# Kernel optimization log

Measured on AMD Instinct MI355X. Metric: run time of the kernel, lower is better.

Reference implementation:

```python
import jax, jax.numpy as jnp
import numpy as np

B, C = 32768, 1000
EPS = 1e-6

def setup_inputs() -> dict:
    key = jax.random.key(0)
    k1, k2 = jax.random.split(key)
    # p_tar / p_vlm are probability distributions over C classes
    p_tar = jax.nn.softmax(jax.random.normal(k1, (B, C), dtype=jnp.float32), axis=1)
    p_vlm = jax.nn.softmax(jax.random.normal(k2, (B, C), dtype=jnp.float32), axis=1)
    alpha = jnp.array([0.99], dtype=jnp.float32)  # EMA momentum
    memory_bank = jnp.full((C, C), 1.0 / C, dtype=jnp.float32)  # __init__ state
    return {"p_tar": p_tar, "p_vlm": p_vlm, "alpha": alpha, "memory_bank": memory_bank}

def _uncertainty(p):
    return -p * jnp.log(p + EPS)

def reference(p_tar, p_vlm, alpha, memory_bank):
    n_classes = memory_bank.shape[0]
    norm = 1.0 / jnp.sqrt(jnp.float32(n_classes))
    # --- class_prototype_atten (uses PRE-update memory bank, as in torch) ---
    atten = jax.nn.softmax(jnp.matmul(p_tar, memory_bank.T) * norm, axis=1)  # [B, C]
    p_tar_new = jnp.matmul(atten, memory_bank)  # [B, C]
    # --- update_membank: vectorized per-class masked-mean EMA ---
    y_tar = jnp.argmax(p_tar, axis=1)
    y_vlm = jnp.argmax(p_vlm, axis=1)
    agree = y_tar == y_vlm
    # non-agreeing rows dumped into extra segment n_classes
    seg = jnp.where(agree, y_tar, n_classes)
    sums = jax.ops.segment_sum(p_tar, seg, num_segments=n_classes + 1)[:n_classes]  # [C, C]
    counts = jax.ops.segment_sum(agree.astype(p_tar.dtype), seg, num_segments=n_classes + 1)[:n_classes]  # [C]
    has = counts > 0
    mean = sums / jnp.where(has, counts, 1.0)[:, None]
    a = alpha.reshape(())
    bank_new = jnp.where(has[:, None], a * memory_bank + (1.0 - a) * mean, memory_bank)
    # --- uncertainty_mixing ---
    eu_tar = jnp.exp(-_uncertainty(p_tar_new))
    eu_vlm = jnp.exp(-_uncertainty(p_vlm))
    p_mix = (eu_tar * p_tar_new + eu_vlm * p_vlm) / (eu_tar + eu_vlm)
    return p_mix, bank_new
```

## Files before the change

### kernel.cpp

```cpp
#include <hip/hip_runtime.h>
#include <hip/hip_bf16.h>
#include <cstdint>
#include <cstddef>

#define NROWS 32768
#define NCLS  1000
#define KP    1024

typedef unsigned short u16;
typedef __bf16 bf16x8 __attribute__((ext_vector_type(8)));
typedef float  f32x4  __attribute__((ext_vector_type(4)));

__device__ __forceinline__ void gld_lds16(const u16* g, u16* l) {
  __builtin_amdgcn_global_load_lds(
      (const __attribute__((address_space(1))) unsigned int*)g,
      (__attribute__((address_space(3))) unsigned int*)l, 16, 0, 0);
}

__global__ void prep_bank(const float* __restrict__ bank,
                          __hip_bfloat16* __restrict__ Mb,
                          __hip_bfloat16* __restrict__ MTb) {
  __shared__ float tile[32][33];
  const int bx = blockIdx.x * 32;
  const int by = blockIdx.y * 32;
  for (int t = threadIdx.y; t < 32; t += 8) {
    int j = by + t, k = bx + threadIdx.x;
    float v = (j < NCLS && k < NCLS) ? bank[j * NCLS + k] : 0.0f;
    Mb[j * KP + k] = __float2bfloat16(v);
    tile[t][threadIdx.x] = v;
  }
  __syncthreads();
  for (int t = threadIdx.y; t < 32; t += 8) {
    int k = bx + t, j = by + threadIdx.x;
    MTb[k * KP + j] = __float2bfloat16(tile[threadIdx.x][t]);
  }
}

__global__ __launch_bounds__(256)
void rows_kernel(const float* __restrict__ p_tar, const float* __restrict__ p_vlm,
                 __hip_bfloat16* __restrict__ Abf,
                 float* __restrict__ sums, float* __restrict__ counts) {
  const int wid  = threadIdx.x >> 6;
  const int lane = threadIdx.x & 63;
  const int row  = blockIdx.x * 4 + wid;
  const float* tr = p_tar + (size_t)row * NCLS;
  const float* vr = p_vlm + (size_t)row * NCLS;
  __hip_bfloat16* ar = Abf + (size_t)row * KP;

  float bvT = -1.0f; int biT = 0;
  for (int c = lane; c < NCLS; c += 64) {
    float v = tr[c];
    ar[c] = __float2bfloat16(v);
    if (v > bvT) { bvT = v; biT = c; }
  }
  if (lane < KP - NCLS) ar[NCLS + lane] = __float2bfloat16(0.0f);

  float bvV = -1.0f; int biV = 0;
  for (int c = lane; c < NCLS; c += 64) {
    float v = vr[c];
    if (v > bvV) { bvV = v; biV = c; }
  }
  #pragma unroll
  for (int d = 1; d < 64; d <<= 1) {
    float ov = __shfl_xor(bvT, d); int oi = __shfl_xor(biT, d);
    if (ov > bvT || (ov == bvT && oi < biT)) { bvT = ov; biT = oi; }
    float ov2 = __shfl_xor(bvV, d); int oi2 = __shfl_xor(biV, d);
    if (ov2 > bvV || (ov2 == bvV && oi2 < biV)) { bvV = ov2; biV = oi2; }
  }
  if (biT == biV) {
    if (lane == 0) atomicAdd(&counts[biT], 1.0f);
    for (int c = lane; c < NCLS; c += 64)
      atomicAdd(&sums[(size_t)biT * NCLS + c], tr[c]);
  }
}

template <int WHICH>
__global__ __launch_bounds__(256)
void gemm_bt(const u16* __restrict__ Amat, const u16* __restrict__ Bmat,
             __hip_bfloat16* __restrict__ Eout,
             const float* __restrict__ rowsum,
             const float* __restrict__ p_vlm,
             float* __restrict__ mix_out) {
  __shared__ u16 As[128 * 32];
  __shared__ u16 Bs[128 * 32];
  const int tid  = threadIdx.x;
  const int wid  = tid >> 6;
  const int lane = tid & 63;
  const int lr   = lane & 15;
  const int q    = lane >> 4;
  const int bm   = blockIdx.y;
  const int bn   = blockIdx.x;
  const int wm   = wid >> 1;
  const int wn   = wid & 1;

  f32x4 acc[4][4] = {};

  const int srow = wid * 32 + (lane >> 2);
  const int skb  = (lane & 3) * 8;
  const u16* ag0 = Amat + (size_t)(bm * 128 + srow) * KP + skb;
  const u16* ag1 = ag0 + (size_t)16 * KP;
  const u16* bg0 = Bmat + (size_t)(bn * 128 + srow) * KP + skb;
  const u16* bg1 = bg0 + (size_t)16 * KP;
  u16* as0 = &As[(wid * 2 + 0) * 512];
  u16* as1 = &As[(wid * 2 + 1) * 512];
  u16* bs0 = &Bs[(wid * 2 + 0) * 512];
  u16* bs1 = &Bs[(wid * 2 + 1) * 512];

  for (int k0 = 0; k0 < KP; k0 += 32) {
    gld_lds16(ag0 + k0, as0);
    gld_lds16(ag1 + k0, as1);
    gld_lds16(bg0 + k0, bs0);
    gld_lds16(bg1 + k0, bs1);
    __syncthreads();

    bf16x8 af[4], bfr[4];
    #pragma unroll
    for (int t = 0; t < 4; ++t) {
      af[t]  = *(const bf16x8*)(&As[(wm * 64 + t * 16 + lr) * 32 + q * 8]);
      bfr[t] = *(const bf16x8*)(&Bs[(wn * 64 + t * 16 + lr) * 32 + q * 8]);
    }
    #pragma unroll
    for (int mt = 0; mt < 4; ++mt)
      #pragma unroll
      for (int nt = 0; nt < 4; ++nt)
        acc[mt][nt] = __builtin_amdgcn_mfma_f32_16x16x32_bf16(af[mt], bfr[nt], acc[mt][nt], 0, 0, 0);
    __syncthreads();
  }

  const float NORM = 0.03162277660168379f;
  #pragma unroll
  for (int mt = 0; mt < 4; ++mt) {
    #pragma unroll
    for (int r = 0; r < 4; ++r) {
      const int gm = bm * 128 + wm * 64 + mt * 16 + q * 4 + r;
      if (WHICH == 1) {
        #pragma unroll
        for (int nt = 0; nt < 4; ++nt) {
          const int gn = bn * 128 + wn * 64 + nt * 16 + lr;
          float e = (gn < NCLS) ? __expf(acc[mt][nt][r] * NORM) : 0.0f;
          Eout[(size_t)gm * KP + gn] = __float2bfloat16(e);
        }
      } else {
        const float inv = 1.0f / rowsum[gm];
        #pragma unroll
        for (int nt = 0; nt < 4; ++nt) {
          const int gn = bn * 128 + wn * 64 + nt * 16 + lr;
          if (gn < NCLS) {
            float pt = acc[mt][nt][r] * inv;
            float pv = p_vlm[(size_t)gm * NCLS + gn];
            float et = __expf(pt * __logf(pt + 1e-6f));
            float ev = __expf(pv * __logf(pv + 1e-6f));
            mix_out[(size_t)gm * NCLS + gn] = (et * pt + ev * pv) / (et + ev);
          }
        }
      }
    }
  }
}

__global__ __launch_bounds__(256)
void rowsum_kernel(const u16* __restrict__ E, float* __restrict__ rs) {
  const int wid  = threadIdx.x >> 6;
  const int lane = threadIdx.x & 63;
  const int row  = blockIdx.x * 4 + wid;
  const u16* er = E + (size_t)row * KP;
  const bf16x8* p = (const bf16x8*)(er + lane * 16);
  bf16x8 v0 = p[0], v1 = p[1];
  float s = 0.0f;
  #pragma unroll
  for (int i = 0; i < 8; ++i) s += (float)v0[i] + (float)v1[i];
  #pragma unroll
  for (int d = 1; d < 64; d <<= 1) s += __shfl_xor(s, d);
  if (lane == 0) rs[row] = s;
}

__global__ __launch_bounds__(256)
void bank_update(const float* __restrict__ bank, const float* __restrict__ sums,
                 const float* __restrict__ counts, const float* __restrict__ alpha,
                 float* __restrict__ out) {
  const int idx = blockIdx.x * 256 + threadIdx.x;
  if (idx >= NCLS * NCLS) return;
  const int r = idx / NCLS;
  const float cnt = counts[r];
  const float bv  = bank[idx];
  const float a   = alpha[0];
  out[idx] = (cnt > 0.0f) ? a * bv + (1.0f - a) * (sums[idx] / cnt) : bv;
}

extern "C" void kernel_launch(void* const* d_in, const int* in_sizes, int n_in,
                              void* d_out, int out_size, void* d_ws, size_t ws_size,
                              hipStream_t stream) {
  const float* p_tar = (const float*)d_in[0];
  const float* p_vlm = (const float*)d_in[1];
  const float* alpha = (const float*)d_in[2];
  const float* bank  = (const float*)d_in[3];
  float* out_mix  = (float*)d_out;
  float* out_bank = (float*)d_out + (size_t)NROWS * NCLS;

  char* w = (char*)d_ws;
  __hip_bfloat16* Abf = (__hip_bfloat16*)w; w += (size_t)NROWS * KP * 2;
  __hip_bfloat16* Ebf = (__hip_bfloat16*)w; w += (size_t)NROWS * KP * 2;
  __hip_bfloat16* Mb  = (__hip_bfloat16*)w; w += (size_t)KP * KP * 2;
  __hip_bfloat16* MTb = (__hip_bfloat16*)w; w += (size_t)KP * KP * 2;
  float* sums   = (float*)w;                w += (size_t)NCLS * NCLS * 4;
  float* counts = (float*)w;                w += 1024 * 4;
  float* rs     = (float*)w;                w += (size_t)NROWS * 4;

  hipMemsetAsync(sums, 0, (size_t)NCLS * NCLS * 4 + 1024 * 4, stream);

  prep_bank<<<dim3(KP / 32, KP / 32), dim3(32, 8), 0, stream>>>(bank, Mb, MTb);
  rows_kernel<<<NROWS / 4, 256, 0, stream>>>(p_tar, p_vlm, Abf, sums, counts);
  gemm_bt<1><<<dim3(KP / 128, NROWS / 128), 256, 0, stream>>>(
      (const u16*)Abf, (const u16*)Mb, Ebf, nullptr, nullptr, nullptr);
  rowsum_kernel<<<NROWS / 4, 256, 0, stream>>>((const u16*)Ebf, rs);
  gemm_bt<2><<<dim3(KP / 128, NROWS / 128), 256, 0, stream>>>(
      (const u16*)Ebf, (const u16*)MTb, nullptr, rs, p_vlm, out_mix);
  bank_update<<<(NCLS * NCLS + 255) / 256, 256, 0, stream>>>(bank, sums, counts, alpha, out_bank);
}
```

Baseline: 675.6 us.

## Double-buffer GEMM LDS tiles, fuse rowsum into GEMM epilogue, vectorize row loads

The GEMM main loop now uses two LDS buffers so the next K-slice is prefetched while MFMAs run on the current one, which drops one barrier per iteration. The softmax row-sum is computed in the first GEMM's epilogue with shuffles and atomics, replacing the separate rowsum kernel and its extra pass over E. Blocks are remapped so consecutive blocks share the same N tile (column-major order), and occupancy is hinted via launch bounds. rows_kernel reads float4 and writes bf16x4 to cut per-element memory transactions. The row-sum atomics make the result order-dependent, and the doubled LDS may limit occupancy.

```diff
diff --git a/kernel.cpp b/kernel.cpp
--- a/kernel.cpp
+++ b/kernel.cpp
@@ -9,6 +9,7 @@
 
 typedef unsigned short u16;
 typedef __bf16 bf16x8 __attribute__((ext_vector_type(8)));
+typedef __bf16 bf16x4 __attribute__((ext_vector_type(4)));
 typedef float  f32x4  __attribute__((ext_vector_type(4)));
 
 __device__ __forceinline__ void gld_lds16(const u16* g, u16* l) {
@@ -45,20 +46,30 @@
   const int row  = blockIdx.x * 4 + wid;
   const float* tr = p_tar + (size_t)row * NCLS;
   const float* vr = p_vlm + (size_t)row * NCLS;
+  const float4* tr4 = (const float4*)tr;
+  const float4* vr4 = (const float4*)vr;
   __hip_bfloat16* ar = Abf + (size_t)row * KP;
 
   float bvT = -1.0f; int biT = 0;
-  for (int c = lane; c < NCLS; c += 64) {
-    float v = tr[c];
-    ar[c] = __float2bfloat16(v);
-    if (v > bvT) { bvT = v; biT = c; }
+  for (int i = lane; i < 250; i += 64) {
+    float4 v = tr4[i];
+    bf16x4 o;
+    o[0] = (__bf16)v.x; o[1] = (__bf16)v.y; o[2] = (__bf16)v.z; o[3] = (__bf16)v.w;
+    ((bf16x4*)ar)[i] = o;
+    if (v.x > bvT) { bvT = v.x; biT = 4 * i; }
+    if (v.y > bvT) { bvT = v.y; biT = 4 * i + 1; }
+    if (v.z > bvT) { bvT = v.z; biT = 4 * i + 2; }
+    if (v.w > bvT) { bvT = v.w; biT = 4 * i + 3; }
   }
   if (lane < KP - NCLS) ar[NCLS + lane] = __float2bfloat16(0.0f);
 
   float bvV = -1.0f; int biV = 0;
-  for (int c = lane; c < NCLS; c += 64) {
-    float v = vr[c];
-    if (v > bvV) { bvV = v; biV = c; }
+  for (int i = lane; i < 250; i += 64) {
+    float4 v = vr4[i];
+    if (v.x > bvV) { bvV = v.x; biV = 4 * i; }
+    if (v.y > bvV) { bvV = v.y; biV = 4 * i + 1; }
+    if (v.z > bvV) { bvV = v.z; biV = 4 * i + 2; }
+    if (v.w > bvV) { bvV = v.w; biV = 4 * i + 3; }
   }
   #pragma unroll
   for (int d = 1; d < 64; d <<= 1) {
@@ -75,23 +86,24 @@
 }
 
 template <int WHICH>
-__global__ __launch_bounds__(256)
+__global__ __launch_bounds__(256, 4)
 void gemm_bt(const u16* __restrict__ Amat, const u16* __restrict__ Bmat,
              __hip_bfloat16* __restrict__ Eout,
-             const float* __restrict__ rowsum,
+             float* __restrict__ rowsum,
              const float* __restrict__ p_vlm,
              float* __restrict__ mix_out) {
-  __shared__ u16 As[128 * 32];
-  __shared__ u16 Bs[128 * 32];
+  __shared__ u16 As[2][128 * 32];
+  __shared__ u16 Bs[2][128 * 32];
   const int tid  = threadIdx.x;
   const int wid  = tid >> 6;
   const int lane = tid & 63;
   const int lr   = lane & 15;
   const int q    = lane >> 4;
-  const int bm   = blockIdx.y;
-  const int bn   = blockIdx.x;
-  const int wm   = wid >> 1;
-  const int wn   = wid & 1;
+  const int L  = blockIdx.y * 8 + blockIdx.x;
+  const int bm = L & 255;
+  const int bn = L >> 8;
+  const int wm = wid >> 1;
+  const int wn = wid & 1;
 
   f32x4 acc[4][4] = {};
 
@@ -101,30 +113,37 @@
   const u16* ag1 = ag0 + (size_t)16 * KP;
   const u16* bg0 = Bmat + (size_t)(bn * 128 + srow) * KP + skb;
   const u16* bg1 = bg0 + (size_t)16 * KP;
-  u16* as0 = &As[(wid * 2 + 0) * 512];
-  u16* as1 = &As[(wid * 2 + 1) * 512];
-  u16* bs0 = &Bs[(wid * 2 + 0) * 512];
-  u16* bs1 = &Bs[(wid * 2 + 1) * 512];
-
-  for (int k0 = 0; k0 < KP; k0 += 32) {
-    gld_lds16(ag0 + k0, as0);
-    gld_lds16(ag1 + k0, as1);
-    gld_lds16(bg0 + k0, bs0);
-    gld_lds16(bg1 + k0, bs1);
+  const int lofs0 = (wid * 2 + 0) * 512;
+  const int lofs1 = (wid * 2 + 1) * 512;
+
+  gld_lds16(ag0, &As[0][lofs0]);
+  gld_lds16(ag1, &As[0][lofs1]);
+  gld_lds16(bg0, &Bs[0][lofs0]);
+  gld_lds16(bg1, &Bs[0][lofs1]);
+
+  const int NITER = KP / 32;
+  for (int i = 0; i < NITER; ++i) {
+    const int cur = i & 1;
     __syncthreads();
-
+    if (i + 1 < NITER) {
+      const int k0 = (i + 1) * 32;
+      const int nxt = cur ^ 1;
+      gld_lds16(ag0 + k0, &As[nxt][lofs0]);
+      gld_lds16(ag1 + k0, &As[nxt][lofs1]);
+      gld_lds16(bg0 + k0, &Bs[nxt][lofs0]);
+      gld_lds16(bg1 + k0, &Bs[nxt][lofs1]);
+    }
     bf16x8 af[4], bfr[4];
     #pragma unroll
     for (int t = 0; t < 4; ++t) {
-      af[t]  = *(const bf16x8*)(&As[(wm * 64 + t * 16 + lr) * 32 + q * 8]);
-      bfr[t] = *(const bf16x8*)(&Bs[(wn * 64 + t * 16 + lr) * 32 + q * 8]);
+      af[t]  = *(const bf16x8*)(&As[cur][(wm * 64 + t * 16 + lr) * 32 + q * 8]);
+      bfr[t] = *(const bf16x8*)(&Bs[cur][(wn * 64 + t * 16 + lr) * 32 + q * 8]);
     }
     #pragma unroll
     for (int mt = 0; mt < 4; ++mt)
       #pragma unroll
       for (int nt = 0; nt < 4; ++nt)
         acc[mt][nt] = __builtin_amdgcn_mfma_f32_16x16x32_bf16(af[mt], bfr[nt], acc[mt][nt], 0, 0, 0);
-    __syncthreads();
   }
 
   const float NORM = 0.03162277660168379f;
@@ -134,12 +153,19 @@
     for (int r = 0; r < 4; ++r) {
       const int gm = bm * 128 + wm * 64 + mt * 16 + q * 4 + r;
       if (WHICH == 1) {
+        float psum = 0.0f;
         #pragma unroll
         for (int nt = 0; nt < 4; ++nt) {
           const int gn = bn * 128 + wn * 64 + nt * 16 + lr;
           float e = (gn < NCLS) ? __expf(acc[mt][nt][r] * NORM) : 0.0f;
           Eout[(size_t)gm * KP + gn] = __float2bfloat16(e);
+          psum += e;
         }
+        psum += __shfl_xor(psum, 1);
+        psum += __shfl_xor(psum, 2);
+        psum += __shfl_xor(psum, 4);
+        psum += __shfl_xor(psum, 8);
+        if (lr == 0) atomicAdd(&rowsum[gm], psum);
       } else {
         const float inv = 1.0f / rowsum[gm];
         #pragma unroll
@@ -159,22 +185,6 @@
 }
 
 __global__ __launch_bounds__(256)
-void rowsum_kernel(const u16* __restrict__ E, float* __restrict__ rs) {
-  const int wid  = threadIdx.x >> 6;
-  const int lane = threadIdx.x & 63;
-  const int row  = blockIdx.x * 4 + wid;
-  const u16* er = E + (size_t)row * KP;
-  const bf16x8* p = (const bf16x8*)(er + lane * 16);
-  bf16x8 v0 = p[0], v1 = p[1];
-  float s = 0.0f;
-  #pragma unroll
-  for (int i = 0; i < 8; ++i) s += (float)v0[i] + (float)v1[i];
-  #pragma unroll
-  for (int d = 1; d < 64; d <<= 1) s += __shfl_xor(s, d);
-  if (lane == 0) rs[row] = s;
-}
-
-__global__ __launch_bounds__(256)
 void bank_update(const float* __restrict__ bank, const float* __restrict__ sums,
                  const float* __restrict__ counts, const float* __restrict__ alpha,
                  float* __restrict__ out) {
@@ -206,13 +216,12 @@
   float* counts = (float*)w;                w += 1024 * 4;
   float* rs     = (float*)w;                w += (size_t)NROWS * 4;
 
-  hipMemsetAsync(sums, 0, (size_t)NCLS * NCLS * 4 + 1024 * 4, stream);
+  hipMemsetAsync(sums, 0, (size_t)NCLS * NCLS * 4 + 1024 * 4 + (size_t)NROWS * 4, stream);
 
   prep_bank<<<dim3(KP / 32, KP / 32), dim3(32, 8), 0, stream>>>(bank, Mb, MTb);
   rows_kernel<<<NROWS / 4, 256, 0, stream>>>(p_tar, p_vlm, Abf, sums, counts);
   gemm_bt<1><<<dim3(KP / 128, NROWS / 128), 256, 0, stream>>>(
-      (const u16*)Abf, (const u16*)Mb, Ebf, nullptr, nullptr, nullptr);
-  rowsum_kernel<<<NROWS / 4, 256, 0, stream>>>((const u16*)Ebf, rs);
+      (const u16*)Abf, (const u16*)Mb, Ebf, rs, nullptr, nullptr);
   gemm_bt<2><<<dim3(KP / 128, NROWS / 128), 256, 0, stream>>>(
       (const u16*)Ebf, (const u16*)MTb, nullptr, rs, p_vlm, out_mix);
   bank_update<<<(NCLS * NCLS + 255) / 256, 256, 0, stream>>>(bank, sums, counts, alpha, out_bank);
```

Result: faster. 603.9 us (-10.6%).

## Pre-tile operands into MFMA fragment layout, double-buffer GEMM, fuse rowsum into epilogue

Applied to the files above, without the earlier changes.

Operands (p_tar, bank, bank^T, and the exp intermediate) are stored in a 16x32 panel-chunk layout matching MFMA fragments, so the GEMM reads contiguous 512-element chunks and LDS reads become linear per lane. The GEMM K-loop is double-buffered with global_load_lds prefetch of the next chunk, and block indices are remapped so blocks sharing a B tile are grouped. The softmax row-sum is accumulated with atomics in the first GEMM's epilogue, which removes the separate rowsum kernel, and the row pass uses vectorized float4 loads. The cost is atomic contention on rowsum plus more complex indexing and staging through LDS in the epilogue.

```diff
diff --git a/kernel.cpp b/kernel.cpp
--- a/kernel.cpp
+++ b/kernel.cpp
@@ -6,10 +6,12 @@
 #define NROWS 32768
 #define NCLS  1000
 #define KP    1024
+#define NCH   32
 
 typedef unsigned short u16;
 typedef __bf16 bf16x8 __attribute__((ext_vector_type(8)));
 typedef float  f32x4  __attribute__((ext_vector_type(4)));
+
 
 __device__ __forceinline__ void gld_lds16(const u16* g, u16* l) {
   __builtin_amdgcn_global_load_lds(
@@ -17,130 +19,202 @@
       (__attribute__((address_space(3))) unsigned int*)l, 16, 0, 0);
 }
 
-__global__ void prep_bank(const float* __restrict__ bank,
-                          __hip_bfloat16* __restrict__ Mb,
-                          __hip_bfloat16* __restrict__ MTb) {
+__global__ __launch_bounds__(128)
+void prep4_bank(const float* __restrict__ bank,
+                __hip_bfloat16* __restrict__ M4,
+                __hip_bfloat16* __restrict__ MT4) {
   __shared__ float tile[32][33];
-  const int bx = blockIdx.x * 32;
-  const int by = blockIdx.y * 32;
-  for (int t = threadIdx.y; t < 32; t += 8) {
-    int j = by + t, k = bx + threadIdx.x;
-    float v = (j < NCLS && k < NCLS) ? bank[j * NCLS + k] : 0.0f;
-    Mb[j * KP + k] = __float2bfloat16(v);
-    tile[t][threadIdx.x] = v;
+  const int tx = blockIdx.x;
+  const int ty = blockIdx.y;
+  const int t  = threadIdx.x;
+  {
+    const int r = t >> 2, c0 = (t & 3) * 8;
+    const int gj = ty * 32 + r;
+    #pragma unroll
+    for (int j = 0; j < 8; ++j) {
+      const int gk = tx * 32 + c0 + j;
+      tile[r][c0 + j] = (gj < NCLS && gk < NCLS) ? bank[gj * NCLS + gk] : 0.0f;
+    }
   }
   __syncthreads();
-  for (int t = threadIdx.y; t < 32; t += 8) {
-    int k = bx + t, j = by + threadIdx.x;
-    MTb[k * KP + j] = __float2bfloat16(tile[threadIdx.x][t]);
+  const int w = t >> 6, lane = t & 63, lr = lane & 15, qq = lane >> 4;
+  if (w == 0) {
+    #pragma unroll
+    for (int s = 0; s < 2; ++s) {
+      bf16x8 o;
+      #pragma unroll
+      for (int j = 0; j < 8; ++j) o[j] = (__bf16)tile[s * 16 + lr][qq * 8 + j];
+      *(bf16x8*)((u16*)M4 + ((size_t)(ty * 2 + s) * NCH + tx) * 512 + lane * 8) = o;
+    }
+  } else {
+    #pragma unroll
+    for (int s = 0; s < 2; ++s) {
+      bf16x8 o;
+      #pragma unroll
+      for (int j = 0; j < 8; ++j) o[j] = (__bf16)tile[qq * 8 + j][s * 16 + lr];
+      *(bf16x8*)((u16*)MT4 + ((size_t)(tx * 2 + s) * NCH + ty) * 512 + lane * 8) = o;
+    }
   }
 }
 
 __global__ __launch_bounds__(256)
-void rows_kernel(const float* __restrict__ p_tar, const float* __restrict__ p_vlm,
-                 __hip_bfloat16* __restrict__ Abf,
-                 float* __restrict__ sums, float* __restrict__ counts) {
-  const int wid  = threadIdx.x >> 6;
-  const int lane = threadIdx.x & 63;
-  const int row  = blockIdx.x * 4 + wid;
+void rows4_kernel(const float* __restrict__ p_tar, const float* __restrict__ p_vlm,
+                  __hip_bfloat16* __restrict__ A4,
+                  float* __restrict__ sums, float* __restrict__ counts) {
+  const int w = threadIdx.x >> 6, lane = threadIdx.x & 63;
+  const int lr = lane & 15, q = lane >> 4;
+  const int panel = blockIdx.x * 4 + w;
+  const int row   = panel * 16 + lr;
   const float* tr = p_tar + (size_t)row * NCLS;
   const float* vr = p_vlm + (size_t)row * NCLS;
-  __hip_bfloat16* ar = Abf + (size_t)row * KP;
+  u16* a4 = (u16*)A4 + (size_t)panel * NCH * 512 + lane * 8;
 
   float bvT = -1.0f; int biT = 0;
-  for (int c = lane; c < NCLS; c += 64) {
-    float v = tr[c];
-    ar[c] = __float2bfloat16(v);
-    if (v > bvT) { bvT = v; biT = c; }
-  }
-  if (lane < KP - NCLS) ar[NCLS + lane] = __float2bfloat16(0.0f);
-
   float bvV = -1.0f; int biV = 0;
-  for (int c = lane; c < NCLS; c += 64) {
-    float v = vr[c];
-    if (v > bvV) { bvV = v; biV = c; }
+  for (int c = 0; c < NCH; ++c) {
+    const int k0 = c * 32 + q * 8;
+    float v[8];
+    if (k0 < NCLS) {
+      float4 x = *(const float4*)(tr + k0);
+      float4 y = *(const float4*)(tr + k0 + 4);
+      v[0] = x.x; v[1] = x.y; v[2] = x.z; v[3] = x.w;
+      v[4] = y.x; v[5] = y.y; v[6] = y.z; v[7] = y.w;
+    } else {
+      #pragma unroll
+      for (int j = 0; j < 8; ++j) v[j] = 0.0f;
+    }
+    bf16x8 o;
+    #pragma unroll
+    for (int j = 0; j < 8; ++j) {
+      o[j] = (__bf16)v[j];
+      if (v[j] > bvT) { bvT = v[j]; biT = k0 + j; }
+    }
+    *(bf16x8*)(a4 + (size_t)c * 512) = o;
+    if (k0 < NCLS) {
+      float4 x = *(const float4*)(vr + k0);
+      float4 y = *(const float4*)(vr + k0 + 4);
+      float u[8] = {x.x, x.y, x.z, x.w, y.x, y.y, y.z, y.w};
+      #pragma unroll
+      for (int j = 0; j < 8; ++j)
+        if (u[j] > bvV) { bvV = u[j]; biV = k0 + j; }
+    }
   }
   #pragma unroll
-  for (int d = 1; d < 64; d <<= 1) {
+  for (int d = 16; d < 64; d <<= 1) {
     float ov = __shfl_xor(bvT, d); int oi = __shfl_xor(biT, d);
     if (ov > bvT || (ov == bvT && oi < biT)) { bvT = ov; biT = oi; }
     float ov2 = __shfl_xor(bvV, d); int oi2 = __shfl_xor(biV, d);
     if (ov2 > bvV || (ov2 == bvV && oi2 < biV)) { bvV = ov2; biV = oi2; }
   }
-  if (biT == biV) {
-    if (lane == 0) atomicAdd(&counts[biT], 1.0f);
-    for (int c = lane; c < NCLS; c += 64)
-      atomicAdd(&sums[(size_t)biT * NCLS + c], tr[c]);
+  const int ag = (biT == biV) ? 1 : 0;
+  for (int rr = 0; rr < 16; ++rr) {
+    const int agr = __shfl(ag, rr);
+    if (agr) {
+      const int cls = __shfl(biT, rr);
+      const float* trr = p_tar + (size_t)(panel * 16 + rr) * NCLS;
+      for (int k = lane; k < NCLS; k += 64)
+        atomicAdd(&sums[(size_t)cls * NCLS + k], trr[k]);
+      if (lane == 0) atomicAdd(&counts[cls], 1.0f);
+    }
   }
 }
 
 template <int WHICH>
-__global__ __launch_bounds__(256)
-void gemm_bt(const u16* __restrict__ Amat, const u16* __restrict__ Bmat,
-             __hip_bfloat16* __restrict__ Eout,
-             const float* __restrict__ rowsum,
-             const float* __restrict__ p_vlm,
-             float* __restrict__ mix_out) {
-  __shared__ u16 As[128 * 32];
-  __shared__ u16 Bs[128 * 32];
+__global__ __launch_bounds__(256, 4)
+void gemm4(const u16* __restrict__ A4, const u16* __restrict__ B4,
+           __hip_bfloat16* __restrict__ E4out, float* __restrict__ rowsum,
+           const float* __restrict__ p_vlm, float* __restrict__ mix_out) {
+  __shared__ u16 SH[4][4096];
   const int tid  = threadIdx.x;
-  const int wid  = tid >> 6;
+  const int w    = tid >> 6;
   const int lane = tid & 63;
   const int lr   = lane & 15;
   const int q    = lane >> 4;
-  const int bm   = blockIdx.y;
-  const int bn   = blockIdx.x;
-  const int wm   = wid >> 1;
-  const int wn   = wid & 1;
+  const int L    = blockIdx.y * 8 + blockIdx.x;
+  const int bm   = L & 255;
+  const int bn   = L >> 8;
+  const int wm   = w >> 1;
+  const int wn   = w & 1;
 
   f32x4 acc[4][4] = {};
 
-  const int srow = wid * 32 + (lane >> 2);
-  const int skb  = (lane & 3) * 8;
-  const u16* ag0 = Amat + (size_t)(bm * 128 + srow) * KP + skb;
-  const u16* ag1 = ag0 + (size_t)16 * KP;
-  const u16* bg0 = Bmat + (size_t)(bn * 128 + srow) * KP + skb;
-  const u16* bg1 = bg0 + (size_t)16 * KP;
-  u16* as0 = &As[(wid * 2 + 0) * 512];
-  u16* as1 = &As[(wid * 2 + 1) * 512];
-  u16* bs0 = &Bs[(wid * 2 + 0) * 512];
-  u16* bs1 = &Bs[(wid * 2 + 1) * 512];
-
-  for (int k0 = 0; k0 < KP; k0 += 32) {
-    gld_lds16(ag0 + k0, as0);
-    gld_lds16(ag1 + k0, as1);
-    gld_lds16(bg0 + k0, bs0);
-    gld_lds16(bg1 + k0, bs1);
+  const u16* ga0 = A4 + ((size_t)(bm * 8 + 2 * w) * NCH) * 512 + lane * 8;
+  const u16* ga1 = ga0 + (size_t)NCH * 512;
+  const u16* gb0 = B4 + ((size_t)(bn * 8 + 2 * w) * NCH) * 512 + lane * 8;
+  const u16* gb1 = gb0 + (size_t)NCH * 512;
+
+  gld_lds16(ga0, &SH[0][(2 * w + 0) * 512]);
+  gld_lds16(ga1, &SH[0][(2 * w + 1) * 512]);
+  gld_lds16(gb0, &SH[2][(2 * w + 0) * 512]);
+  gld_lds16(gb1, &SH[2][(2 * w + 1) * 512]);
+
+  for (int i = 0; i < NCH; ++i) {
+    const int cur = i & 1;
     __syncthreads();
-
+    if (i + 1 < NCH) {
+      const int nxt = cur ^ 1;
+      const size_t ko = (size_t)(i + 1) * 512;
+      gld_lds16(ga0 + ko, &SH[nxt][(2 * w + 0) * 512]);
+      gld_lds16(ga1 + ko, &SH[nxt][(2 * w + 1) * 512]);
+      gld_lds16(gb0 + ko, &SH[2 + nxt][(2 * w + 0) * 512]);
+      gld_lds16(gb1 + ko, &SH[2 + nxt][(2 * w + 1) * 512]);
+    }
     bf16x8 af[4], bfr[4];
     #pragma unroll
     for (int t = 0; t < 4; ++t) {
-      af[t]  = *(const bf16x8*)(&As[(wm * 64 + t * 16 + lr) * 32 + q * 8]);
-      bfr[t] = *(const bf16x8*)(&Bs[(wn * 64 + t * 16 + lr) * 32 + q * 8]);
+      af[t]  = *(const bf16x8*)(&SH[cur][(wm * 4 + t) * 512 + lane * 8]);
+      bfr[t] = *(const bf16x8*)(&SH[2 + cur][(wn * 4 + t) * 512 + lane * 8]);
     }
     #pragma unroll
     for (int mt = 0; mt < 4; ++mt)
       #pragma unroll
       for (int nt = 0; nt < 4; ++nt)
         acc[mt][nt] = __builtin_amdgcn_mfma_f32_16x16x32_bf16(af[mt], bfr[nt], acc[mt][nt], 0, 0, 0);
+  }
+
+  const float NORM = 0.03162277660168379f;
+  if (WHICH == 1) {
     __syncthreads();
-  }
-
-  const float NORM = 0.03162277660168379f;
-  #pragma unroll
-  for (int mt = 0; mt < 4; ++mt) {
-    #pragma unroll
-    for (int r = 0; r < 4; ++r) {
-      const int gm = bm * 128 + wm * 64 + mt * 16 + q * 4 + r;
-      if (WHICH == 1) {
+    u16* ep = &SH[w][0];
+    #pragma unroll
+    for (int mt = 0; mt < 4; ++mt) {
+      float psum[4] = {0.f, 0.f, 0.f, 0.f};
+      #pragma unroll
+      for (int nt = 0; nt < 4; ++nt) {
+        const int gn = bn * 128 + wn * 64 + nt * 16 + lr;
+        const int cc = nt >> 1;
+        const int q2 = (nt & 1) * 2 + (lr >> 3);
+        const int jj = lr & 7;
         #pragma unroll
-        for (int nt = 0; nt < 4; ++nt) {
-          const int gn = bn * 128 + wn * 64 + nt * 16 + lr;
+        for (int r = 0; r < 4; ++r) {
           float e = (gn < NCLS) ? __expf(acc[mt][nt][r] * NORM) : 0.0f;
-          Eout[(size_t)gm * KP + gn] = __float2bfloat16(e);
+          psum[r] += e;
+          __hip_bfloat16 h = __float2bfloat16(e);
+          ep[(mt * 2 + cc) * 512 + (q2 * 16 + q * 4 + r) * 8 + jj] = *(u16*)&h;
         }
-      } else {
+      }
+      #pragma unroll
+      for (int r = 0; r < 4; ++r) {
+        float s = psum[r];
+        s += __shfl_xor(s, 1); s += __shfl_xor(s, 2);
+        s += __shfl_xor(s, 4); s += __shfl_xor(s, 8);
+        if (lr == 0) atomicAdd(&rowsum[bm * 128 + wm * 64 + mt * 16 + q * 4 + r], s);
+      }
+    }
+    #pragma unroll
+    for (int ch = 0; ch < 8; ++ch) {
+      const int mt = ch >> 1, cc = ch & 1;
+      bf16x8 v = *(const bf16x8*)(&ep[ch * 512 + lane * 8]);
+      const size_t Rg = bm * 8 + wm * 4 + mt;
+      const size_t cg = bn * 4 + wn * 2 + cc;
+      *(bf16x8*)((u16*)E4out + (Rg * NCH + cg) * 512 + lane * 8) = v;
+    }
+  } else {
+    #pragma unroll
+    for (int mt = 0; mt < 4; ++mt) {
+      #pragma unroll
+      for (int r = 0; r < 4; ++r) {
+        const int gm = bm * 128 + wm * 64 + mt * 16 + q * 4 + r;
         const float inv = 1.0f / rowsum[gm];
         #pragma unroll
         for (int nt = 0; nt < 4; ++nt) {
@@ -159,22 +233,6 @@
 }
 
 __global__ __launch_bounds__(256)
-void rowsum_kernel(const u16* __restrict__ E, float* __restrict__ rs) {
-  const int wid  = threadIdx.x >> 6;
-  const int lane = threadIdx.x & 63;
-  const int row  = blockIdx.x * 4 + wid;
-  const u16* er = E + (size_t)row * KP;
-  const bf16x8* p = (const bf16x8*)(er + lane * 16);
-  bf16x8 v0 = p[0], v1 = p[1];
-  float s = 0.0f;
-  #pragma unroll
-  for (int i = 0; i < 8; ++i) s += (float)v0[i] + (float)v1[i];
-  #pragma unroll
-  for (int d = 1; d < 64; d <<= 1) s += __shfl_xor(s, d);
-  if (lane == 0) rs[row] = s;
-}
-
-__global__ __launch_bounds__(256)
 void bank_update(const float* __restrict__ bank, const float* __restrict__ sums,
                  const float* __restrict__ counts, const float* __restrict__ alpha,
                  float* __restrict__ out) {
@@ -198,22 +256,21 @@
   float* out_bank = (float*)d_out + (size_t)NROWS * NCLS;
 
   char* w = (char*)d_ws;
-  __hip_bfloat16* Abf = (__hip_bfloat16*)w; w += (size_t)NROWS * KP * 2;
-  __hip_bfloat16* Ebf = (__hip_bfloat16*)w; w += (size_t)NROWS * KP * 2;
-  __hip_bfloat16* Mb  = (__hip_bfloat16*)w; w += (size_t)KP * KP * 2;
-  __hip_bfloat16* MTb = (__hip_bfloat16*)w; w += (size_t)KP * KP * 2;
+  __hip_bfloat16* A4  = (__hip_bfloat16*)w; w += (size_t)NROWS * KP * 2;
+  __hip_bfloat16* E4  = (__hip_bfloat16*)w; w += (size_t)NROWS * KP * 2;
+  __hip_bfloat16* M4  = (__hip_bfloat16*)w; w += (size_t)KP * KP * 2;
+  __hip_bfloat16* MT4 = (__hip_bfloat16*)w; w += (size_t)KP * KP * 2;
   float* sums   = (float*)w;                w += (size_t)NCLS * NCLS * 4;
   float* counts = (float*)w;                w += 1024 * 4;
   float* rs     = (float*)w;                w += (size_t)NROWS * 4;
 
-  hipMemsetAsync(sums, 0, (size_t)NCLS * NCLS * 4 + 1024 * 4, stream);
-
-  prep_bank<<<dim3(KP / 32, KP / 32), dim3(32, 8), 0, stream>>>(bank, Mb, MTb);
-  rows_kernel<<<NROWS / 4, 256, 0, stream>>>(p_tar, p_vlm, Abf, sums, counts);
-  gemm_bt<1><<<dim3(KP / 128, NROWS / 128), 256, 0, stream>>>(
-      (const u16*)Abf, (const u16*)Mb, Ebf, nullptr, nullptr, nullptr);
-  rowsum_kernel<<<NROWS / 4, 256, 0, stream>>>((const u16*)Ebf, rs);
-  gemm_bt<2><<<dim3(KP / 128, NROWS / 128), 256, 0, stream>>>(
-      (const u16*)Ebf, (const u16*)MTb, nullptr, rs, p_vlm, out_mix);
+  hipMemsetAsync(sums, 0, (size_t)NCLS * NCLS * 4 + 1024 * 4 + (size_t)NROWS * 4, stream);
+
+  prep4_bank<<<dim3(32, 32), 128, 0, stream>>>(bank, M4, MT4);
+  rows4_kernel<<<NROWS / 64, 256, 0, stream>>>(p_tar, p_vlm, A4, sums, counts);
+  gemm4<1><<<dim3(8, 256), 256, 0, stream>>>(
+      (const u16*)A4, (const u16*)M4, E4, rs, nullptr, nullptr);
+  gemm4<2><<<dim3(8, 256), 256, 0, stream>>>(
+      (const u16*)E4, (const u16*)MT4, nullptr, rs, p_vlm, out_mix);
   bank_update<<<(NCLS * NCLS + 255) / 256, 256, 0, stream>>>(bank, sums, counts, alpha, out_bank);
 }
```

After: 597.4 us. 11.6% less time.
